# Performance work log

Measured on AMD Instinct MI355X. Metric: run time of the kernel, lower is better.

Reference implementation:

```python
import jax, jax.numpy as jnp
import numpy as np

LN_EPS = 1e-5


def setup_inputs() -> dict:
    key = jax.random.key(0)
    ks = jax.random.split(key, 3)
    B, C, H, W = 2, 256, 64, 64
    x = jax.random.normal(ks[0], (B, C, H, W), dtype=jnp.float32)
    ln_gamma = jnp.ones((C,), dtype=jnp.float32)
    ln_beta = jnp.zeros((C,), dtype=jnp.float32)
    w_qkv = jax.random.normal(ks[1], (3 * C, C), dtype=jnp.float32) * 0.02
    w_proj = jax.random.normal(ks[2], (C, C), dtype=jnp.float32) * 0.02
    b_proj = jnp.zeros((C,), dtype=jnp.float32)
    return {"x": x, "ln_gamma": ln_gamma, "ln_beta": ln_beta,
            "w_qkv": w_qkv, "w_proj": w_proj, "b_proj": b_proj}


def reference(x, ln_gamma, ln_beta, w_qkv, w_proj, b_proj):
    B, C, H, W = x.shape
    num_heads = 8
    head_dim = C // num_heads
    scale = head_dim ** -0.5

    # patch2token: B C H W -> B N C
    t = x.reshape(B, C, H * W).transpose(0, 2, 1)
    res = t

    # LayerNorm over channel dim
    mu = t.mean(-1, keepdims=True)
    var = t.var(-1, keepdims=True)
    tn = (t - mu) * jax.lax.rsqrt(var + LN_EPS) * ln_gamma + ln_beta

    # qkv projection (torch Linear: y = x @ W.T)
    N = H * W
    qkv = jnp.einsum('bnc,oc->bno', tn, w_qkv)  # B N 3C
    qkv = qkv.reshape(B, N, 3, num_heads, head_dim).transpose(2, 0, 3, 1, 4)
    q, k, v = qkv[0], qkv[1], qkv[2]  # each B h N d

    attn = jnp.einsum('bhnd,bhmd->bhnm', q, k) * scale  # B h N N
    attn = jax.nn.softmax(attn, axis=-1)
    out = jnp.einsum('bhnm,bhmd->bhnd', attn, v)  # B h N d
    out = out.transpose(0, 2, 1, 3).reshape(B, N, C)

    out = jnp.einsum('bnc,oc->bno', out, w_proj) + b_proj
    out = res + out

    # token2patch: B N C -> B C H W
    return out.transpose(0, 2, 1).reshape(B, C, H, W)
```

## Files before the change

kernel.cpp:

```cpp
#include <hip/hip_runtime.h>

typedef __bf16 bf16x8 __attribute__((ext_vector_type(8)));
typedef float f32x16 __attribute__((ext_vector_type(16)));
typedef unsigned int uint4v __attribute__((ext_vector_type(4)));
typedef unsigned int uint2v __attribute__((ext_vector_type(2)));
typedef unsigned short u16;

#define MFMA32(a, b, c) __builtin_amdgcn_mfma_f32_32x32x16_bf16((a), (b), (c), 0, 0, 0)

static __device__ __forceinline__ u16 f2bf(float f) {
  unsigned u = __builtin_bit_cast(unsigned, f);
  u += 0x7fffu + ((u >> 16) & 1u);
  return (u16)(u >> 16);
}

static __device__ __forceinline__ f32x16 zero16() {
  f32x16 z;
#pragma unroll
  for (int i = 0; i < 16; ++i) z[i] = 0.0f;
  return z;
}


__global__ __launch_bounds__(256) void convw_kernel(
    const float* __restrict__ wq, const float* __restrict__ wp,
    u16* __restrict__ wqf, u16* __restrict__ wpf) {
  int t = threadIdx.x;
  int u = (blockIdx.x << 2) + (t >> 6);
  int l = t & 63, lo = l & 31, hi = l >> 5;
  const float* src; u16* dst; int ot, s;
  if (u < 384) { ot = u >> 4; s = u & 15; src = wq; dst = wqf; }
  else { int u2 = u - 384; ot = u2 >> 4; s = u2 & 15; src = wp; dst = wpf; }
  const float* p = src + (ot * 32 + lo) * 256 + s * 16 + 8 * hi;
  bf16x8 f;
#pragma unroll
  for (int i = 0; i < 8; ++i) f[i] = (__bf16)p[i];
  *(bf16x8*)(dst + (ot * 16 + s) * 512 + l * 8) = f;
}

__global__ __launch_bounds__(256) void prepqkv_kernel(
    const float* __restrict__ x, const float* __restrict__ gamma,
    const float* __restrict__ beta, const u16* __restrict__ wqf,
    u16* __restrict__ qg, u16* __restrict__ kf, u16* __restrict__ vf) {
  __shared__ float xs[32][257];
  __shared__ float red[2][8][32];
  __shared__ float mu_s[32], rs_s[32];
  __shared__ float gs[256], bs[256];
  __shared__ u16 af[16 * 512];
  __shared__ u16 lsb[4][32][32];
  int t = threadIdx.x;
  int mt = blockIdx.x;
  int n0g = mt * 32;
  int b = n0g >> 12, nn = n0g & 4095;
  int ni = t & 31, g = t >> 5;
  gs[t] = gamma[t]; bs[t] = beta[t];
  float s1 = 0.f, s2 = 0.f;
  for (int c = g; c < 256; c += 8) {
    float v = x[(((b << 8) + c) << 12) + nn + ni];
    xs[ni][c] = v;
    s1 += v; s2 += v * v;
  }
  red[0][g][ni] = s1; red[1][g][ni] = s2;
  __syncthreads();
  if (t < 32) {
    float ss = 0.f, qq = 0.f;
#pragma unroll
    for (int k = 0; k < 8; ++k) { ss += red[0][k][t]; qq += red[1][k][t]; }
    float mean = ss * (1.f / 256.f);
    float var = qq * (1.f / 256.f) - mean * mean;
    mu_s[t] = mean;
    rs_s[t] = rsqrtf(var + 1e-5f);
  }
  __syncthreads();
  int l = t & 63, w = t >> 6, lo = l & 31, hi = l >> 5;
  {
    float mu = mu_s[lo], rs = rs_s[lo];
#pragma unroll
    for (int jj = 0; jj < 4; ++jj) {
      int s = w * 4 + jj;
      bf16x8 f;
#pragma unroll
      for (int i = 0; i < 8; ++i) {
        int c = s * 16 + 8 * hi + i;
        f[i] = (__bf16)((xs[lo][c] - mu) * rs * gs[c] + bs[c]);
      }
      *(bf16x8*)(af + s * 512 + l * 8) = f;
    }
  }
  __syncthreads();

  bf16x8 ar[16];
#pragma unroll
  for (int s = 0; s < 16; ++s) ar[s] = *(const bf16x8*)(af + s * 512 + l * 8);
  const float sl2e = 0.17677669529663688f * 1.4426950408889634f;
  int bb = n0g >> 12, n0 = n0g & 4095;
  int tt = n0 >> 5;
#pragma unroll
  for (int oi = 0; oi < 6; ++oi) {
    int ot = w * 6 + oi;
    int o0 = ot * 32;
    f32x16 acc = zero16();
    const bf16x8* bp = (const bf16x8*)(wqf + (ot * 16) * 512 + l * 8);
#pragma unroll
    for (int s = 0; s < 16; ++s) acc = MFMA32(ar[s], bp[s * 64], acc);
    int sec = o0 >> 8;
    int hh = (o0 & 255) >> 5;
    float mul = (sec == 0) ? sl2e : 1.0f;
    if (sec == 2) {
#pragma unroll
      for (int r = 0; r < 16; ++r) {
        int row = (r & 3) + 8 * (r >> 2) + 4 * hi;
        lsb[w][lo][row] = f2bf(acc[r]);
      }
    } else {
#pragma unroll
      for (int r = 0; r < 16; ++r) {
        int row = (r & 3) + 8 * (r >> 2) + 4 * hi;
        lsb[w][row][lo] = f2bf(acc[r] * mul);
      }
    }
    int bh = (bb << 3) + hh;
    if (sec == 0) {
      u16* dst = qg + (((bh << 12) + n0 + (l >> 1)) << 5) + (l & 1) * 16;
      const u16* srow = &lsb[w][l >> 1][(l & 1) * 16];
      *(uint4v*)(dst) = *(const uint4v*)(srow);
      *(uint4v*)(dst + 8) = *(const uint4v*)(srow + 8);
    } else {
      u16* base = (sec == 1) ? kf : vf;
      u16* dst = base + ((bh * 128 + tt) * 2) * 512 + l * 8;
      *(uint4v*)(dst) = *(const uint4v*)&lsb[w][lo][8 * hi];
      *(uint4v*)(dst + 512) = *(const uint4v*)&lsb[w][lo][16 + 8 * hi];
    }
  }
}

__global__ __launch_bounds__(512) void attn_proj_kernel(
    const u16* __restrict__ qg, const u16* __restrict__ kf,
    const u16* __restrict__ vf, const u16* __restrict__ wpf,
    const float* __restrict__ bpj, const float* __restrict__ x,
    float* __restrict__ out) {
  __shared__ u16 ls_all[8][32][32];
  __shared__ float lsf[8][32][33];
  int t = threadIdx.x;
  int l = t & 63, w = t >> 6, lo = l & 31, hi = l >> 5;
  int b = blockIdx.x >> 7, qt = blockIdx.x & 127;
  int bh = (b << 3) + w;
  const u16* qp = qg + (((bh << 12) + qt * 32 + lo) << 5);
  bf16x8 qf0 = *(const bf16x8*)(qp + hi * 8);
  bf16x8 qf1 = *(const bf16x8*)(qp + 16 + hi * 8);
  const u16* kfb = kf + (size_t)bh * 131072 + l * 8;
  const u16* vfb = vf + (size_t)bh * 131072 + l * 8;
  const f32x16 zf = zero16();
  f32x16 oacc = zero16();
  f32x16 lacc = zero16();
  const uint4v onesu = {0x3F803F80u, 0x3F803F80u, 0x3F803F80u, 0x3F803F80u};
  const bf16x8 ones8 = __builtin_bit_cast(bf16x8, onesu);

#define LOADT(T, K0, K1, V0, V1) do {                  \
    const u16* kq_ = kfb + (T) * 1024;                 \
    const u16* vq_ = vfb + (T) * 1024;                 \
    K0 = *(const bf16x8*)(kq_);                        \
    K1 = *(const bf16x8*)(kq_ + 512);                  \
    V0 = *(const bf16x8*)(vq_);                        \
    V1 = *(const bf16x8*)(vq_ + 512);                  \
  } while (0)

#define ABODY(K0, K1, V0, V1) do {                                          \
    f32x16 sa = MFMA32(K0, qf0, zf);                                        \
    sa = MFMA32(K1, qf1, sa);                                               \
    f32x16 tmag = sa * 128.0f + 8404864.0f;                                 \
    unsigned pk[8];                                                         \
    _Pragma("unroll")                                                       \
    for (int j = 0; j < 8; ++j) {                                           \
      pk[j] = __builtin_amdgcn_perm(                                        \
          __builtin_bit_cast(unsigned, tmag[2 * j + 1]),                    \
          __builtin_bit_cast(unsigned, tmag[2 * j]), 0x05040100u);          \
    }                                                                       \
    uint2v A0 = __builtin_amdgcn_permlane32_swap(pk[0], pk[2], false, false); \
    uint2v A1 = __builtin_amdgcn_permlane32_swap(pk[1], pk[3], false, false); \
    uint2v B0 = __builtin_amdgcn_permlane32_swap(pk[4], pk[6], false, false); \
    uint2v B1 = __builtin_amdgcn_permlane32_swap(pk[5], pk[7], false, false); \
    uint4v u0v = {A0[0], A1[0], A0[1], A1[1]};                              \
    uint4v u1v = {B0[0], B1[0], B0[1], B1[1]};                              \
    bf16x8 p0 = __builtin_bit_cast(bf16x8, u0v);                            \
    bf16x8 p1 = __builtin_bit_cast(bf16x8, u1v);                            \
    __builtin_amdgcn_s_setprio(1);                                          \
    oacc = MFMA32(V0, p0, oacc);                                            \
    lacc = MFMA32(ones8, p0, lacc);                                         \
    oacc = MFMA32(V1, p1, oacc);                                            \
    lacc = MFMA32(ones8, p1, lacc);                                         \
    __builtin_amdgcn_s_setprio(0);                                          \
  } while (0)

  bf16x8 ak0, ak1, av0, av1, bk0, bk1, bv0, bv1;
  LOADT(0, ak0, ak1, av0, av1);
  LOADT(1, bk0, bk1, bv0, bv1);
  for (int tt = 0; tt < 128; tt += 2) {
    bf16x8 ck0, ck1, cv0, cv1, dk0, dk1, dv0, dv1;
    if (tt + 2 < 128) LOADT(tt + 2, ck0, ck1, cv0, cv1);
    ABODY(ak0, ak1, av0, av1);
    if (tt + 3 < 128) LOADT(tt + 3, dk0, dk1, dv0, dv1);
    ABODY(bk0, bk1, bv0, bv1);
    ak0 = ck0; ak1 = ck1; av0 = cv0; av1 = cv1;
    bk0 = dk0; bk1 = dk1; bv0 = dv0; bv1 = dv1;
  }
#undef LOADT
#undef ABODY

  float inv = 1.0f / lacc[0];
#pragma unroll
  for (int r = 0; r < 16; ++r) {
    int row = (r & 3) + 8 * (r >> 2) + 4 * hi;
    ls_all[w][lo][row] = f2bf(oacc[r] * inv);
  }
  __syncthreads();

  f32x16 acc = zero16();
  const bf16x8* bp = (const bf16x8*)(wpf + (w * 16) * 512 + l * 8);
#pragma unroll
  for (int s = 0; s < 16; ++s) {
    bf16x8 af = *(const bf16x8*)&ls_all[s >> 1][lo][(s & 1) * 16 + 8 * hi];
    acc = MFMA32(af, bp[s * 64], acc);
  }
  int c0 = w * 32;
  float bias = bpj[c0 + lo];
#pragma unroll
  for (int r = 0; r < 16; ++r) {
    int row = (r & 3) + 8 * (r >> 2) + 4 * hi;
    lsf[w][row][lo] = acc[r] + bias;
  }
  int n0 = qt * 32;
#pragma unroll
  for (int r2 = 0; r2 < 16; ++r2) {
    int cl = 2 * r2 + hi;
    int idx = (((b << 8) + c0 + cl) << 12) + n0 + lo;
    out[idx] = lsf[w][lo][cl] + x[idx];
  }
}

extern "C" void kernel_launch(void* const* d_in, const int* in_sizes, int n_in,
                              void* d_out, int out_size, void* d_ws, size_t ws_size,
                              hipStream_t stream) {
  const float* x      = (const float*)d_in[0];
  const float* gamma  = (const float*)d_in[1];
  const float* beta   = (const float*)d_in[2];
  const float* w_qkv  = (const float*)d_in[3];
  const float* w_proj = (const float*)d_in[4];
  const float* b_proj = (const float*)d_in[5];
  float* out = (float*)d_out;
  char* ws = (char*)d_ws;
  const size_t MB = 1024 * 1024;
  u16* qg  = (u16*)(ws);
  u16* kf  = (u16*)(ws + 4 * MB);
  u16* vf  = (u16*)(ws + 8 * MB);
  u16* wqf = (u16*)(ws + 12 * MB);
  u16* wpf = (u16*)(ws + 12 * MB + 768 * 256 * sizeof(u16));

  hipLaunchKernelGGL(convw_kernel, dim3(128), dim3(256), 0, stream,
                     w_qkv, w_proj, wqf, wpf);
  hipLaunchKernelGGL(prepqkv_kernel, dim3(256), dim3(256), 0, stream,
                     x, gamma, beta, wqf, qg, kf, vf);
  hipLaunchKernelGGL(attn_proj_kernel, dim3(256), dim3(512), 0, stream,
                     qg, kf, vf, wpf, b_proj, x, out);
}
```

Baseline: 141.3 us.

## Fuse three kernels into one cooperative kernel with grid-wide syncs

Merges the weight conversion, LayerNorm+QKV projection, and attention+output projection kernels into a single cooperative launch of 256 blocks of 512 threads, separated by grid.sync barriers. The aim is to remove two kernel launch boundaries and their gaps. The price is grid-sync overhead, a 512-thread shape for the QKV stage (fewer output tiles per wave), and a large shared memory union that may limit occupancy. Cooperative launch also requires all 256 blocks to be co-resident.

After: 199.0 us. +40.8%, slower.

```diff
diff --git a/kernel.cpp b/kernel.cpp
--- a/kernel.cpp
+++ b/kernel.cpp
@@ -1,4 +1,7 @@
 #include <hip/hip_runtime.h>
+#include <hip/hip_cooperative_groups.h>
+
+namespace cg = cooperative_groups;
 
 typedef __bf16 bf16x8 __attribute__((ext_vector_type(8)));
 typedef float f32x16 __attribute__((ext_vector_type(16)));
@@ -21,140 +24,142 @@
   return z;
 }
 
-
-__global__ __launch_bounds__(256) void convw_kernel(
-    const float* __restrict__ wq, const float* __restrict__ wp,
-    u16* __restrict__ wqf, u16* __restrict__ wpf) {
+__global__ __launch_bounds__(512) void fused_kernel(
+    const float* __restrict__ x, const float* __restrict__ gamma,
+    const float* __restrict__ beta, const float* __restrict__ wq,
+    const float* __restrict__ wp, const float* __restrict__ bpj,
+    u16* __restrict__ wqf, u16* __restrict__ wpf,
+    u16* __restrict__ qg, u16* __restrict__ kf, u16* __restrict__ vf,
+    float* __restrict__ out) {
+  __shared__ __align__(16) char smem[55680];
+  float (*xs)[257] = reinterpret_cast<float (*)[257]>(smem);
+  u16* af          = reinterpret_cast<u16*>(smem + 32896);
+  float (*red)[16][32] = reinterpret_cast<float (*)[16][32]>(smem + 49280);
+  float* mu_s = reinterpret_cast<float*>(smem + 53376);
+  float* rs_s = reinterpret_cast<float*>(smem + 53504);
+  float* gs   = reinterpret_cast<float*>(smem + 53632);
+  float* bs   = reinterpret_cast<float*>(smem + 54656);
+  u16 (*lsb)[32][32] = reinterpret_cast<u16 (*)[32][32]>(smem);
+  u16 (*ls_all)[32][32] = reinterpret_cast<u16 (*)[32][32]>(smem);
+  float (*lsf)[32][33] = reinterpret_cast<float (*)[32][33]>(smem + 16384);
+
+  cg::grid_group grid = cg::this_grid();
   int t = threadIdx.x;
-  int u = (blockIdx.x << 2) + (t >> 6);
-  int l = t & 63, lo = l & 31, hi = l >> 5;
-  const float* src; u16* dst; int ot, s;
-  if (u < 384) { ot = u >> 4; s = u & 15; src = wq; dst = wqf; }
-  else { int u2 = u - 384; ot = u2 >> 4; s = u2 & 15; src = wp; dst = wpf; }
-  const float* p = src + (ot * 32 + lo) * 256 + s * 16 + 8 * hi;
-  bf16x8 f;
-#pragma unroll
-  for (int i = 0; i < 8; ++i) f[i] = (__bf16)p[i];
-  *(bf16x8*)(dst + (ot * 16 + s) * 512 + l * 8) = f;
-}
-
-__global__ __launch_bounds__(256) void prepqkv_kernel(
-    const float* __restrict__ x, const float* __restrict__ gamma,
-    const float* __restrict__ beta, const u16* __restrict__ wqf,
-    u16* __restrict__ qg, u16* __restrict__ kf, u16* __restrict__ vf) {
-  __shared__ float xs[32][257];
-  __shared__ float red[2][8][32];
-  __shared__ float mu_s[32], rs_s[32];
-  __shared__ float gs[256], bs[256];
-  __shared__ u16 af[16 * 512];
-  __shared__ u16 lsb[4][32][32];
-  int t = threadIdx.x;
-  int mt = blockIdx.x;
-  int n0g = mt * 32;
-  int b = n0g >> 12, nn = n0g & 4095;
-  int ni = t & 31, g = t >> 5;
-  gs[t] = gamma[t]; bs[t] = beta[t];
-  float s1 = 0.f, s2 = 0.f;
-  for (int c = g; c < 256; c += 8) {
-    float v = x[(((b << 8) + c) << 12) + nn + ni];
-    xs[ni][c] = v;
-    s1 += v; s2 += v * v;
+  int bid = blockIdx.x;
+  int l = t & 63, w = t >> 6, lo = l & 31, hi = l >> 5;
+
+  if (w < 2) {
+    int u = (bid << 1) + w;
+    const float* src; u16* dst; int ot, s;
+    if (u < 384) { ot = u >> 4; s = u & 15; src = wq; dst = wqf; }
+    else { int u2 = u - 384; ot = u2 >> 4; s = u2 & 15; src = wp; dst = wpf; }
+    const float* p = src + (ot * 32 + lo) * 256 + s * 16 + 8 * hi;
+    bf16x8 f;
+#pragma unroll
+    for (int i = 0; i < 8; ++i) f[i] = (__bf16)p[i];
+    *(bf16x8*)(dst + (ot * 16 + s) * 512 + l * 8) = f;
   }
-  red[0][g][ni] = s1; red[1][g][ni] = s2;
-  __syncthreads();
-  if (t < 32) {
-    float ss = 0.f, qq = 0.f;
-#pragma unroll
-    for (int k = 0; k < 8; ++k) { ss += red[0][k][t]; qq += red[1][k][t]; }
-    float mean = ss * (1.f / 256.f);
-    float var = qq * (1.f / 256.f) - mean * mean;
-    mu_s[t] = mean;
-    rs_s[t] = rsqrtf(var + 1e-5f);
+  grid.sync();
+
+  {
+    int mt = bid;
+    int n0g = mt * 32;
+    int bb = n0g >> 12, nn = n0g & 4095;
+    int ni = t & 31, g = t >> 5;
+    if (t < 256) { gs[t] = gamma[t]; bs[t] = beta[t]; }
+    float s1 = 0.f, s2 = 0.f;
+    for (int c = g; c < 256; c += 16) {
+      float v = x[(((bb << 8) + c) << 12) + nn + ni];
+      xs[ni][c] = v;
+      s1 += v; s2 += v * v;
+    }
+    red[0][g][ni] = s1; red[1][g][ni] = s2;
+    __syncthreads();
+    if (t < 32) {
+      float ss = 0.f, qq = 0.f;
+#pragma unroll
+      for (int k = 0; k < 16; ++k) { ss += red[0][k][t]; qq += red[1][k][t]; }
+      float mean = ss * (1.f / 256.f);
+      float var = qq * (1.f / 256.f) - mean * mean;
+      mu_s[t] = mean;
+      rs_s[t] = rsqrtf(var + 1e-5f);
+    }
+    __syncthreads();
+    {
+      float mu = mu_s[lo], rs = rs_s[lo];
+#pragma unroll
+      for (int jj = 0; jj < 2; ++jj) {
+        int s = w * 2 + jj;
+        bf16x8 f;
+#pragma unroll
+        for (int i = 0; i < 8; ++i) {
+          int c = s * 16 + 8 * hi + i;
+          f[i] = (__bf16)((xs[lo][c] - mu) * rs * gs[c] + bs[c]);
+        }
+        *(bf16x8*)(af + s * 512 + l * 8) = f;
+      }
+    }
+    __syncthreads();
+
+    bf16x8 ar[16];
+#pragma unroll
+    for (int s = 0; s < 16; ++s) ar[s] = *(const bf16x8*)(af + s * 512 + l * 8);
+    const float sl2e = 0.17677669529663688f * 1.4426950408889634f;
+    int n0 = n0g & 4095;
+    int tt = n0 >> 5;
+#pragma unroll
+    for (int oi = 0; oi < 3; ++oi) {
+      int ot = w * 3 + oi;
+      int o0 = ot * 32;
+      f32x16 acc = zero16();
+      const bf16x8* bp = (const bf16x8*)(wqf + (ot * 16) * 512 + l * 8);
+#pragma unroll
+      for (int s = 0; s < 16; ++s) acc = MFMA32(ar[s], bp[s * 64], acc);
+      int sec = o0 >> 8;
+      int hh = (o0 & 255) >> 5;
+      float mul = (sec == 0) ? sl2e : 1.0f;
+      if (sec == 2) {
+#pragma unroll
+        for (int r = 0; r < 16; ++r) {
+          int row = (r & 3) + 8 * (r >> 2) + 4 * hi;
+          lsb[w][lo][row] = f2bf(acc[r]);
+        }
+      } else {
+#pragma unroll
+        for (int r = 0; r < 16; ++r) {
+          int row = (r & 3) + 8 * (r >> 2) + 4 * hi;
+          lsb[w][row][lo] = f2bf(acc[r] * mul);
+        }
+      }
+      int bh = (bb << 3) + hh;
+      if (sec == 0) {
+        u16* dst = qg + (((bh << 12) + n0 + (l >> 1)) << 5) + (l & 1) * 16;
+        const u16* srow = &lsb[w][l >> 1][(l & 1) * 16];
+        *(uint4v*)(dst) = *(const uint4v*)(srow);
+        *(uint4v*)(dst + 8) = *(const uint4v*)(srow + 8);
+      } else {
+        u16* base = (sec == 1) ? kf : vf;
+        u16* dst = base + ((bh * 128 + tt) * 2) * 512 + l * 8;
+        *(uint4v*)(dst) = *(const uint4v*)&lsb[w][lo][8 * hi];
+        *(uint4v*)(dst + 512) = *(const uint4v*)&lsb[w][lo][16 + 8 * hi];
+      }
+    }
   }
-  __syncthreads();
-  int l = t & 63, w = t >> 6, lo = l & 31, hi = l >> 5;
+  grid.sync();
+
   {
-    float mu = mu_s[lo], rs = rs_s[lo];
-#pragma unroll
-    for (int jj = 0; jj < 4; ++jj) {
-      int s = w * 4 + jj;
-      bf16x8 f;
-#pragma unroll
-      for (int i = 0; i < 8; ++i) {
-        int c = s * 16 + 8 * hi + i;
-        f[i] = (__bf16)((xs[lo][c] - mu) * rs * gs[c] + bs[c]);
-      }
-      *(bf16x8*)(af + s * 512 + l * 8) = f;
-    }
-  }
-  __syncthreads();
-
-  bf16x8 ar[16];
-#pragma unroll
-  for (int s = 0; s < 16; ++s) ar[s] = *(const bf16x8*)(af + s * 512 + l * 8);
-  const float sl2e = 0.17677669529663688f * 1.4426950408889634f;
-  int bb = n0g >> 12, n0 = n0g & 4095;
-  int tt = n0 >> 5;
-#pragma unroll
-  for (int oi = 0; oi < 6; ++oi) {
-    int ot = w * 6 + oi;
-    int o0 = ot * 32;
-    f32x16 acc = zero16();
-    const bf16x8* bp = (const bf16x8*)(wqf + (ot * 16) * 512 + l * 8);
-#pragma unroll
-    for (int s = 0; s < 16; ++s) acc = MFMA32(ar[s], bp[s * 64], acc);
-    int sec = o0 >> 8;
-    int hh = (o0 & 255) >> 5;
-    float mul = (sec == 0) ? sl2e : 1.0f;
-    if (sec == 2) {
-#pragma unroll
-      for (int r = 0; r < 16; ++r) {
-        int row = (r & 3) + 8 * (r >> 2) + 4 * hi;
-        lsb[w][lo][row] = f2bf(acc[r]);
-      }
-    } else {
-#pragma unroll
-      for (int r = 0; r < 16; ++r) {
-        int row = (r & 3) + 8 * (r >> 2) + 4 * hi;
-        lsb[w][row][lo] = f2bf(acc[r] * mul);
-      }
-    }
-    int bh = (bb << 3) + hh;
-    if (sec == 0) {
-      u16* dst = qg + (((bh << 12) + n0 + (l >> 1)) << 5) + (l & 1) * 16;
-      const u16* srow = &lsb[w][l >> 1][(l & 1) * 16];
-      *(uint4v*)(dst) = *(const uint4v*)(srow);
-      *(uint4v*)(dst + 8) = *(const uint4v*)(srow + 8);
-    } else {
-      u16* base = (sec == 1) ? kf : vf;
-      u16* dst = base + ((bh * 128 + tt) * 2) * 512 + l * 8;
-      *(uint4v*)(dst) = *(const uint4v*)&lsb[w][lo][8 * hi];
-      *(uint4v*)(dst + 512) = *(const uint4v*)&lsb[w][lo][16 + 8 * hi];
-    }
-  }
-}
-
-__global__ __launch_bounds__(512) void attn_proj_kernel(
-    const u16* __restrict__ qg, const u16* __restrict__ kf,
-    const u16* __restrict__ vf, const u16* __restrict__ wpf,
-    const float* __restrict__ bpj, const float* __restrict__ x,
-    float* __restrict__ out) {
-  __shared__ u16 ls_all[8][32][32];
-  __shared__ float lsf[8][32][33];
-  int t = threadIdx.x;
-  int l = t & 63, w = t >> 6, lo = l & 31, hi = l >> 5;
-  int b = blockIdx.x >> 7, qt = blockIdx.x & 127;
-  int bh = (b << 3) + w;
-  const u16* qp = qg + (((bh << 12) + qt * 32 + lo) << 5);
-  bf16x8 qf0 = *(const bf16x8*)(qp + hi * 8);
-  bf16x8 qf1 = *(const bf16x8*)(qp + 16 + hi * 8);
-  const u16* kfb = kf + (size_t)bh * 131072 + l * 8;
-  const u16* vfb = vf + (size_t)bh * 131072 + l * 8;
-  const f32x16 zf = zero16();
-  f32x16 oacc = zero16();
-  f32x16 lacc = zero16();
-  const uint4v onesu = {0x3F803F80u, 0x3F803F80u, 0x3F803F80u, 0x3F803F80u};
-  const bf16x8 ones8 = __builtin_bit_cast(bf16x8, onesu);
+    int b = bid >> 7, qt = bid & 127;
+    int bh = (b << 3) + w;
+    const u16* qp = qg + (((bh << 12) + qt * 32 + lo) << 5);
+    bf16x8 qf0 = *(const bf16x8*)(qp + hi * 8);
+    bf16x8 qf1 = *(const bf16x8*)(qp + 16 + hi * 8);
+    const u16* kfb = kf + (size_t)bh * 131072 + l * 8;
+    const u16* vfb = vf + (size_t)bh * 131072 + l * 8;
+    const f32x16 zf = zero16();
+    f32x16 oacc = zero16();
+    f32x16 lacc = zero16();
+    const uint4v onesu = {0x3F803F80u, 0x3F803F80u, 0x3F803F80u, 0x3F803F80u};
+    const bf16x8 ones8 = __builtin_bit_cast(bf16x8, onesu);
 
 #define LOADT(T, K0, K1, V0, V1) do {                  \
     const u16* kq_ = kfb + (T) * 1024;                 \
@@ -192,49 +197,50 @@
     __builtin_amdgcn_s_setprio(0);                                          \
   } while (0)
 
-  bf16x8 ak0, ak1, av0, av1, bk0, bk1, bv0, bv1;
-  LOADT(0, ak0, ak1, av0, av1);
-  LOADT(1, bk0, bk1, bv0, bv1);
-  for (int tt = 0; tt < 128; tt += 2) {
-    bf16x8 ck0, ck1, cv0, cv1, dk0, dk1, dv0, dv1;
-    if (tt + 2 < 128) LOADT(tt + 2, ck0, ck1, cv0, cv1);
-    ABODY(ak0, ak1, av0, av1);
-    if (tt + 3 < 128) LOADT(tt + 3, dk0, dk1, dv0, dv1);
-    ABODY(bk0, bk1, bv0, bv1);
-    ak0 = ck0; ak1 = ck1; av0 = cv0; av1 = cv1;
-    bk0 = dk0; bk1 = dk1; bv0 = dv0; bv1 = dv1;
-  }
+    bf16x8 ak0, ak1, av0, av1, bk0, bk1, bv0, bv1;
+    LOADT(0, ak0, ak1, av0, av1);
+    LOADT(1, bk0, bk1, bv0, bv1);
+    for (int tt = 0; tt < 128; tt += 2) {
+      bf16x8 ck0, ck1, cv0, cv1, dk0, dk1, dv0, dv1;
+      if (tt + 2 < 128) LOADT(tt + 2, ck0, ck1, cv0, cv1);
+      ABODY(ak0, ak1, av0, av1);
+      if (tt + 3 < 128) LOADT(tt + 3, dk0, dk1, dv0, dv1);
+      ABODY(bk0, bk1, bv0, bv1);
+      ak0 = ck0; ak1 = ck1; av0 = cv0; av1 = cv1;
+      bk0 = dk0; bk1 = dk1; bv0 = dv0; bv1 = dv1;
+    }
 #undef LOADT
 #undef ABODY
 
-  float inv = 1.0f / lacc[0];
-#pragma unroll
-  for (int r = 0; r < 16; ++r) {
-    int row = (r & 3) + 8 * (r >> 2) + 4 * hi;
-    ls_all[w][lo][row] = f2bf(oacc[r] * inv);
-  }
-  __syncthreads();
-
-  f32x16 acc = zero16();
-  const bf16x8* bp = (const bf16x8*)(wpf + (w * 16) * 512 + l * 8);
-#pragma unroll
-  for (int s = 0; s < 16; ++s) {
-    bf16x8 af = *(const bf16x8*)&ls_all[s >> 1][lo][(s & 1) * 16 + 8 * hi];
-    acc = MFMA32(af, bp[s * 64], acc);
-  }
-  int c0 = w * 32;
-  float bias = bpj[c0 + lo];
-#pragma unroll
-  for (int r = 0; r < 16; ++r) {
-    int row = (r & 3) + 8 * (r >> 2) + 4 * hi;
-    lsf[w][row][lo] = acc[r] + bias;
-  }
-  int n0 = qt * 32;
-#pragma unroll
-  for (int r2 = 0; r2 < 16; ++r2) {
-    int cl = 2 * r2 + hi;
-    int idx = (((b << 8) + c0 + cl) << 12) + n0 + lo;
-    out[idx] = lsf[w][lo][cl] + x[idx];
+    float inv = 1.0f / lacc[0];
+#pragma unroll
+    for (int r = 0; r < 16; ++r) {
+      int row = (r & 3) + 8 * (r >> 2) + 4 * hi;
+      ls_all[w][lo][row] = f2bf(oacc[r] * inv);
+    }
+    __syncthreads();
+
+    f32x16 acc = zero16();
+    const bf16x8* bp = (const bf16x8*)(wpf + (w * 16) * 512 + l * 8);
+#pragma unroll
+    for (int s = 0; s < 16; ++s) {
+      bf16x8 afr = *(const bf16x8*)&ls_all[s >> 1][lo][(s & 1) * 16 + 8 * hi];
+      acc = MFMA32(afr, bp[s * 64], acc);
+    }
+    int c0 = w * 32;
+    float bias = bpj[c0 + lo];
+#pragma unroll
+    for (int r = 0; r < 16; ++r) {
+      int row = (r & 3) + 8 * (r >> 2) + 4 * hi;
+      lsf[w][row][lo] = acc[r] + bias;
+    }
+    int n0 = qt * 32;
+#pragma unroll
+    for (int r2 = 0; r2 < 16; ++r2) {
+      int cl = 2 * r2 + hi;
+      int idx = (((b << 8) + c0 + cl) << 12) + n0 + lo;
+      out[idx] = lsf[w][lo][cl] + x[idx];
+    }
   }
 }
 
@@ -256,10 +262,11 @@
   u16* wqf = (u16*)(ws + 12 * MB);
   u16* wpf = (u16*)(ws + 12 * MB + 768 * 256 * sizeof(u16));
 
-  hipLaunchKernelGGL(convw_kernel, dim3(128), dim3(256), 0, stream,
-                     w_qkv, w_proj, wqf, wpf);
-  hipLaunchKernelGGL(prepqkv_kernel, dim3(256), dim3(256), 0, stream,
-                     x, gamma, beta, wqf, qg, kf, vf);
-  hipLaunchKernelGGL(attn_proj_kernel, dim3(256), dim3(512), 0, stream,
-                     qg, kf, vf, wpf, b_proj, x, out);
-}
+  void* args[] = {
+    (void*)&x, (void*)&gamma, (void*)&beta, (void*)&w_qkv, (void*)&w_proj,
+    (void*)&b_proj, (void*)&wqf, (void*)&wpf, (void*)&qg, (void*)&kf,
+    (void*)&vf, (void*)&out
+  };
+  hipLaunchCooperativeKernel((const void*)fused_kernel, dim3(256), dim3(512),
+                             args, 0, stream);
+}
```

## Switch Q/K/V and attention MFMAs from bf16 to fp8

Applied to the files above, without the earlier changes.

Q, K and V are now stored as fp8 instead of bf16, and both attention MFMA stages (QK^T and PV, plus the row-sum MFMA) use the fp8 32x32x16 instruction. The exp2 bit-trick is re-tuned so that the probabilities land directly in fp8 bit patterns, with the softmax scale folded into a new constant. This halves the K/V bytes streamed per tile and doubles the K per MFMA, aiming to cut memory traffic and matrix-core time in the attention loop. The cost is a large loss of precision in Q, K, V and the probabilities, along with a coarser exp approximation, which may push the output past accuracy tolerance.

After: 128.0 us. 1.1x faster.

```diff
diff --git a/kernel.cpp b/kernel.cpp
--- a/kernel.cpp
+++ b/kernel.cpp
@@ -4,9 +4,12 @@
 typedef float f32x16 __attribute__((ext_vector_type(16)));
 typedef unsigned int uint4v __attribute__((ext_vector_type(4)));
 typedef unsigned int uint2v __attribute__((ext_vector_type(2)));
+typedef long long2v __attribute__((ext_vector_type(2)));
 typedef unsigned short u16;
+typedef unsigned char u8;
 
 #define MFMA32(a, b, c) __builtin_amdgcn_mfma_f32_32x32x16_bf16((a), (b), (c), 0, 0, 0)
+#define MFMA8(a, b, c) __builtin_amdgcn_mfma_f32_32x32x16_fp8_fp8((a), (b), (c), 0, 0, 0)
 
 static __device__ __forceinline__ u16 f2bf(float f) {
   unsigned u = __builtin_bit_cast(unsigned, f);
@@ -41,22 +44,22 @@
 __global__ __launch_bounds__(256) void prepqkv_kernel(
     const float* __restrict__ x, const float* __restrict__ gamma,
     const float* __restrict__ beta, const u16* __restrict__ wqf,
-    u16* __restrict__ qg, u16* __restrict__ kf, u16* __restrict__ vf) {
+    u8* __restrict__ qgf, u8* __restrict__ kgf, u8* __restrict__ vgf) {
   __shared__ float xs[32][257];
   __shared__ float red[2][8][32];
   __shared__ float mu_s[32], rs_s[32];
   __shared__ float gs[256], bs[256];
   __shared__ u16 af[16 * 512];
-  __shared__ u16 lsb[4][32][32];
+  __shared__ u8 ls8[4][32][32];
   int t = threadIdx.x;
   int mt = blockIdx.x;
   int n0g = mt * 32;
-  int b = n0g >> 12, nn = n0g & 4095;
+  int bb = n0g >> 12, nn = n0g & 4095;
   int ni = t & 31, g = t >> 5;
   gs[t] = gamma[t]; bs[t] = beta[t];
   float s1 = 0.f, s2 = 0.f;
   for (int c = g; c < 256; c += 8) {
-    float v = x[(((b << 8) + c) << 12) + nn + ni];
+    float v = x[(((bb << 8) + c) << 12) + nn + ni];
     xs[ni][c] = v;
     s1 += v; s2 += v * v;
   }
@@ -92,8 +95,7 @@
   bf16x8 ar[16];
 #pragma unroll
   for (int s = 0; s < 16; ++s) ar[s] = *(const bf16x8*)(af + s * 512 + l * 8);
-  const float sl2e = 0.17677669529663688f * 1.4426950408889634f;
-  int bb = n0g >> 12, n0 = n0g & 4095;
+  int n0 = n0g & 4095;
   int tt = n0 >> 5;
 #pragma unroll
   for (int oi = 0; oi < 6; ++oi) {
@@ -105,38 +107,37 @@
     for (int s = 0; s < 16; ++s) acc = MFMA32(ar[s], bp[s * 64], acc);
     int sec = o0 >> 8;
     int hh = (o0 & 255) >> 5;
-    float mul = (sec == 0) ? sl2e : 1.0f;
     if (sec == 2) {
 #pragma unroll
-      for (int r = 0; r < 16; ++r) {
-        int row = (r & 3) + 8 * (r >> 2) + 4 * hi;
-        lsb[w][lo][row] = f2bf(acc[r]);
+      for (int j = 0; j < 8; ++j) {
+        int rr = 2 * j;
+        int row = (rr & 3) + 8 * (rr >> 2) + 4 * hi;
+        int pk2 = __builtin_amdgcn_cvt_pk_fp8_f32(acc[rr], acc[rr + 1], 0, false);
+        *(u16*)&ls8[w][lo][row] = (u16)pk2;
       }
     } else {
 #pragma unroll
-      for (int r = 0; r < 16; ++r) {
-        int row = (r & 3) + 8 * (r >> 2) + 4 * hi;
-        lsb[w][row][lo] = f2bf(acc[r] * mul);
+      for (int j = 0; j < 8; ++j) {
+        int rr = 2 * j;
+        int row = (rr & 3) + 8 * (rr >> 2) + 4 * hi;
+        int pk2 = __builtin_amdgcn_cvt_pk_fp8_f32(acc[rr], acc[rr + 1], 0, false);
+        ls8[w][row][lo] = (u8)pk2;
+        ls8[w][row + 1][lo] = (u8)(pk2 >> 8);
       }
     }
+    unsigned long long w0 = *(const unsigned long long*)&ls8[w][lo][hi * 8];
+    unsigned long long w1 = *(const unsigned long long*)&ls8[w][lo][16 + hi * 8];
     int bh = (bb << 3) + hh;
-    if (sec == 0) {
-      u16* dst = qg + (((bh << 12) + n0 + (l >> 1)) << 5) + (l & 1) * 16;
-      const u16* srow = &lsb[w][l >> 1][(l & 1) * 16];
-      *(uint4v*)(dst) = *(const uint4v*)(srow);
-      *(uint4v*)(dst + 8) = *(const uint4v*)(srow + 8);
-    } else {
-      u16* base = (sec == 1) ? kf : vf;
-      u16* dst = base + ((bh * 128 + tt) * 2) * 512 + l * 8;
-      *(uint4v*)(dst) = *(const uint4v*)&lsb[w][lo][8 * hi];
-      *(uint4v*)(dst + 512) = *(const uint4v*)&lsb[w][lo][16 + 8 * hi];
-    }
+    u8* base = (sec == 0) ? qgf : ((sec == 1) ? kgf : vgf);
+    u8* dst = base + (((size_t)bh * 128 + tt) << 10) + l * 16;
+    ((unsigned long long*)dst)[0] = w0;
+    ((unsigned long long*)dst)[1] = w1;
   }
 }
 
 __global__ __launch_bounds__(512) void attn_proj_kernel(
-    const u16* __restrict__ qg, const u16* __restrict__ kf,
-    const u16* __restrict__ vf, const u16* __restrict__ wpf,
+    const u8* __restrict__ qgf, const u8* __restrict__ kgf,
+    const u8* __restrict__ vgf, const u16* __restrict__ wpf,
     const float* __restrict__ bpj, const float* __restrict__ x,
     float* __restrict__ out) {
   __shared__ u16 ls_all[8][32][32];
@@ -145,64 +146,80 @@
   int l = t & 63, w = t >> 6, lo = l & 31, hi = l >> 5;
   int b = blockIdx.x >> 7, qt = blockIdx.x & 127;
   int bh = (b << 3) + w;
-  const u16* qp = qg + (((bh << 12) + qt * 32 + lo) << 5);
-  bf16x8 qf0 = *(const bf16x8*)(qp + hi * 8);
-  bf16x8 qf1 = *(const bf16x8*)(qp + 16 + hi * 8);
-  const u16* kfb = kf + (size_t)bh * 131072 + l * 8;
-  const u16* vfb = vf + (size_t)bh * 131072 + l * 8;
+  long2v qf = *(const long2v*)(qgf + (((size_t)bh * 128 + qt) << 10) + l * 16);
+  const u8* kfb = kgf + (size_t)bh * 131072 + l * 16;
+  const u8* vfb = vgf + (size_t)bh * 131072 + l * 16;
   const f32x16 zf = zero16();
   f32x16 oacc = zero16();
   f32x16 lacc = zero16();
-  const uint4v onesu = {0x3F803F80u, 0x3F803F80u, 0x3F803F80u, 0x3F803F80u};
-  const bf16x8 ones8 = __builtin_bit_cast(bf16x8, onesu);
-
-#define LOADT(T, K0, K1, V0, V1) do {                  \
-    const u16* kq_ = kfb + (T) * 1024;                 \
-    const u16* vq_ = vfb + (T) * 1024;                 \
-    K0 = *(const bf16x8*)(kq_);                        \
-    K1 = *(const bf16x8*)(kq_ + 512);                  \
-    V0 = *(const bf16x8*)(vq_);                        \
-    V1 = *(const bf16x8*)(vq_ + 512);                  \
+  const long ONES8 = 0x3838383838383838L;
+  const float C1 = 8.0f * 0.17677669529663688f * 1.4426950408889634f;
+  const float C2 = 8388664.0f;
+
+#define LOADT(T, KK, VV) do {                          \
+    KK = *(const long2v*)(kfb + (T) * 1024);           \
+    VV = *(const long2v*)(vfb + (T) * 1024);           \
   } while (0)
 
-#define ABODY(K0, K1, V0, V1) do {                                          \
-    f32x16 sa = MFMA32(K0, qf0, zf);                                        \
-    sa = MFMA32(K1, qf1, sa);                                               \
-    f32x16 tmag = sa * 128.0f + 8404864.0f;                                 \
-    unsigned pk[8];                                                         \
-    _Pragma("unroll")                                                       \
-    for (int j = 0; j < 8; ++j) {                                           \
-      pk[j] = __builtin_amdgcn_perm(                                        \
-          __builtin_bit_cast(unsigned, tmag[2 * j + 1]),                    \
-          __builtin_bit_cast(unsigned, tmag[2 * j]), 0x05040100u);          \
+#define ABODY(KK, VV) do {                                                  \
+    f32x16 sa = MFMA8(KK[0], qf[0], zf);                                    \
+    sa = MFMA8(KK[1], qf[1], sa);                                           \
+    f32x16 tm = sa * C1 + C2;                                               \
+    unsigned QA, QB, QC, QD;                                                \
+    {                                                                       \
+      unsigned ya, yb;                                                      \
+      ya = __builtin_amdgcn_perm(__builtin_bit_cast(unsigned, tm[1]),       \
+                                 __builtin_bit_cast(unsigned, tm[0]),       \
+                                 0x00000400u);                              \
+      yb = __builtin_amdgcn_perm(__builtin_bit_cast(unsigned, tm[3]),       \
+                                 __builtin_bit_cast(unsigned, tm[2]),       \
+                                 0x00000400u);                              \
+      QA = __builtin_amdgcn_perm(yb, ya, 0x05040100u);                      \
+      ya = __builtin_amdgcn_perm(__builtin_bit_cast(unsigned, tm[5]),       \
+                                 __builtin_bit_cast(unsigned, tm[4]),       \
+                                 0x00000400u);                              \
+      yb = __builtin_amdgcn_perm(__builtin_bit_cast(unsigned, tm[7]),       \
+                                 __builtin_bit_cast(unsigned, tm[6]),       \
+                                 0x00000400u);                              \
+      QB = __builtin_amdgcn_perm(yb, ya, 0x05040100u);                      \
+      ya = __builtin_amdgcn_perm(__builtin_bit_cast(unsigned, tm[9]),       \
+                                 __builtin_bit_cast(unsigned, tm[8]),       \
+                                 0x00000400u);                              \
+      yb = __builtin_amdgcn_perm(__builtin_bit_cast(unsigned, tm[11]),      \
+                                 __builtin_bit_cast(unsigned, tm[10]),      \
+                                 0x00000400u);                              \
+      QC = __builtin_amdgcn_perm(yb, ya, 0x05040100u);                      \
+      ya = __builtin_amdgcn_perm(__builtin_bit_cast(unsigned, tm[13]),      \
+                                 __builtin_bit_cast(unsigned, tm[12]),      \
+                                 0x00000400u);                              \
+      yb = __builtin_amdgcn_perm(__builtin_bit_cast(unsigned, tm[15]),      \
+                                 __builtin_bit_cast(unsigned, tm[14]),      \
+                                 0x00000400u);                              \
+      QD = __builtin_amdgcn_perm(yb, ya, 0x05040100u);                      \
     }                                                                       \
-    uint2v A0 = __builtin_amdgcn_permlane32_swap(pk[0], pk[2], false, false); \
-    uint2v A1 = __builtin_amdgcn_permlane32_swap(pk[1], pk[3], false, false); \
-    uint2v B0 = __builtin_amdgcn_permlane32_swap(pk[4], pk[6], false, false); \
-    uint2v B1 = __builtin_amdgcn_permlane32_swap(pk[5], pk[7], false, false); \
-    uint4v u0v = {A0[0], A1[0], A0[1], A1[1]};                              \
-    uint4v u1v = {B0[0], B1[0], B0[1], B1[1]};                              \
-    bf16x8 p0 = __builtin_bit_cast(bf16x8, u0v);                            \
-    bf16x8 p1 = __builtin_bit_cast(bf16x8, u1v);                            \
+    uint2v P1 = __builtin_amdgcn_permlane32_swap(QA, QB, false, false);     \
+    uint2v P2 = __builtin_amdgcn_permlane32_swap(QC, QD, false, false);     \
+    long b1 = (long)(((unsigned long long)P1[1] << 32) | P1[0]);            \
+    long b2 = (long)(((unsigned long long)P2[1] << 32) | P2[0]);            \
     __builtin_amdgcn_s_setprio(1);                                          \
-    oacc = MFMA32(V0, p0, oacc);                                            \
-    lacc = MFMA32(ones8, p0, lacc);                                         \
-    oacc = MFMA32(V1, p1, oacc);                                            \
-    lacc = MFMA32(ones8, p1, lacc);                                         \
+    oacc = MFMA8(VV[0], b1, oacc);                                          \
+    lacc = MFMA8(ONES8, b1, lacc);                                          \
+    oacc = MFMA8(VV[1], b2, oacc);                                          \
+    lacc = MFMA8(ONES8, b2, lacc);                                          \
     __builtin_amdgcn_s_setprio(0);                                          \
   } while (0)
 
-  bf16x8 ak0, ak1, av0, av1, bk0, bk1, bv0, bv1;
-  LOADT(0, ak0, ak1, av0, av1);
-  LOADT(1, bk0, bk1, bv0, bv1);
+  long2v ak, av, bk, bv;
+  LOADT(0, ak, av);
+  LOADT(1, bk, bv);
   for (int tt = 0; tt < 128; tt += 2) {
-    bf16x8 ck0, ck1, cv0, cv1, dk0, dk1, dv0, dv1;
-    if (tt + 2 < 128) LOADT(tt + 2, ck0, ck1, cv0, cv1);
-    ABODY(ak0, ak1, av0, av1);
-    if (tt + 3 < 128) LOADT(tt + 3, dk0, dk1, dv0, dv1);
-    ABODY(bk0, bk1, bv0, bv1);
-    ak0 = ck0; ak1 = ck1; av0 = cv0; av1 = cv1;
-    bk0 = dk0; bk1 = dk1; bv0 = dv0; bv1 = dv1;
+    long2v ck, cv, dk, dv;
+    if (tt + 2 < 128) LOADT(tt + 2, ck, cv);
+    ABODY(ak, av);
+    if (tt + 3 < 128) LOADT(tt + 3, dk, dv);
+    ABODY(bk, bv);
+    ak = ck; av = cv;
+    bk = dk; bv = dv;
   }
 #undef LOADT
 #undef ABODY
@@ -219,8 +236,8 @@
   const bf16x8* bp = (const bf16x8*)(wpf + (w * 16) * 512 + l * 8);
 #pragma unroll
   for (int s = 0; s < 16; ++s) {
-    bf16x8 af = *(const bf16x8*)&ls_all[s >> 1][lo][(s & 1) * 16 + 8 * hi];
-    acc = MFMA32(af, bp[s * 64], acc);
+    bf16x8 afr = *(const bf16x8*)&ls_all[s >> 1][lo][(s & 1) * 16 + 8 * hi];
+    acc = MFMA32(afr, bp[s * 64], acc);
   }
   int c0 = w * 32;
   float bias = bpj[c0 + lo];
@@ -250,16 +267,16 @@
   float* out = (float*)d_out;
   char* ws = (char*)d_ws;
   const size_t MB = 1024 * 1024;
-  u16* qg  = (u16*)(ws);
-  u16* kf  = (u16*)(ws + 4 * MB);
-  u16* vf  = (u16*)(ws + 8 * MB);
-  u16* wqf = (u16*)(ws + 12 * MB);
-  u16* wpf = (u16*)(ws + 12 * MB + 768 * 256 * sizeof(u16));
+  u8*  qgf = (u8*)(ws);
+  u8*  kgf = (u8*)(ws + 2 * MB);
+  u8*  vgf = (u8*)(ws + 4 * MB);
+  u16* wqf = (u16*)(ws + 6 * MB);
+  u16* wpf = (u16*)(ws + 6 * MB + 768 * 256 * sizeof(u16));
 
   hipLaunchKernelGGL(convw_kernel, dim3(128), dim3(256), 0, stream,
                      w_qkv, w_proj, wqf, wpf);
   hipLaunchKernelGGL(prepqkv_kernel, dim3(256), dim3(256), 0, stream,
-                     x, gamma, beta, wqf, qg, kf, vf);
+                     x, gamma, beta, wqf, qgf, kgf, vgf);
   hipLaunchKernelGGL(attn_proj_kernel, dim3(256), dim3(512), 0, stream,
-                     qg, kf, vf, wpf, b_proj, x, out);
-}
+                     qgf, kgf, vgf, wpf, b_proj, x, out);
+}
```
